# Performance work log

Hardware: AMD Instinct MI355X
Metric: run time of the kernel (lower is better)

Reference implementation:

```python
import jax, jax.numpy as jnp
import numpy as np

G = 16          # num graphs (equal-size contiguous segments)
P = 500         # kde_grid_points
Q = 20          # num quantiles, np.linspace(0,1,20)
SQRT2PI = float(np.sqrt(2.0 * np.pi))


def _gcn(x, src, dst, W, b):
    # PyG GCNConv: add self-loops, symmetric D^-1/2 (A+I) D^-1/2 aggregation.
    N = x.shape[0]
    xw = x @ W
    deg = jax.ops.segment_sum(jnp.ones_like(src, dtype=x.dtype), dst, num_segments=N) + 1.0
    dinv = jax.lax.rsqrt(deg)
    msg = xw[src] * (dinv[src] * dinv[dst])[:, None]            # [E, D]
    agg = jax.ops.segment_sum(msg, dst, num_segments=N) + xw * (dinv * dinv)[:, None]
    return agg + b


def _att_pool(x, Wg, bg):
    # GlobalAttention: softmax(gate_nn(x)) per graph, weighted sum of x.
    xg = x.reshape(G, -1, x.shape[-1])                          # [G, n, D]
    a = jax.nn.softmax(xg @ Wg + bg, axis=1)                    # [G, n, 1]
    return jnp.sum(a * xg, axis=1)                              # [G, D]


def _kde(xg):
    # xg: [n, D] nodes of one graph -> [D*Q] soft quantile features.
    quant = jnp.linspace(0.0, 1.0, Q, dtype=xg.dtype)
    n = xg.shape[0]
    mn = xg.min(axis=0) - 1e-6
    mx = xg.max(axis=0) + 1e-6
    grid = jnp.linspace(0.0, 1.0, P, dtype=xg.dtype)[:, None] * (mx - mn) + mn   # [P, D]
    std = xg.std(axis=0) + 1e-8 / 3                              # unbiased=False
    h = 1.06 * std * n ** (-0.2)                                 # Silverman bandwidth
    u = (grid[:, None, :] - xg[None, :, :]) / h                  # [P, n, D]
    kern = jnp.exp(-0.5 * u * u) / (h * SQRT2PI)
    dens = kern.mean(axis=1)                                     # [P, D]
    cdf = jnp.cumsum(dens, axis=0)
    cdf = cdf / jnp.clip(cdf[-1:], 1e-8)
    dist = jnp.abs(cdf[:, :, None] - quant)                      # [P, D, Q]
    w = jax.nn.sigmoid(-100.0 * dist)
    w = w / (w.sum(axis=0, keepdims=True) + 1e-8)
    return jnp.sum(grid[:, :, None] * w, axis=0).reshape(-1)     # [D*Q]


def setup_inputs() -> dict:
    key = jax.random.key(0)
    ks = jax.random.split(key, 26)
    N, E, D_in, D_h, D_out = 2048, 32768, 64, 64, 16
    rn = lambda k, s: jax.random.normal(k, s, jnp.float32) * 0.1
    return {
        'x': jax.random.normal(ks[0], (N, D_in), jnp.float32),
        'edge_index': jax.random.randint(ks[1], (2, E), 0, N),
        'gcn_W0': rn(ks[2], (D_in, D_h)), 'gcn_b0': rn(ks[3], (D_h,)),
        'gcn_W1': rn(ks[4], (D_h, D_h)), 'gcn_b1': rn(ks[5], (D_h,)),
        'lp_W0': rn(ks[6], (D_in, D_out)), 'lp_b0': rn(ks[7], (D_out,)),
        'lp_W1': rn(ks[8], (D_h, D_out)), 'lp_b1': rn(ks[9], (D_out,)),
        'cls_W': rn(ks[10], (D_h, D_out)), 'cls_b': rn(ks[11], (D_out,)),
        'kp_W0': rn(ks[12], (D_in * Q, D_out)), 'kp_b0': rn(ks[13], (D_out,)),
        'kp_W1': rn(ks[14], (D_h * Q, D_out)), 'kp_b1': rn(ks[15], (D_out,)),
        'gate_W0': rn(ks[16], (D_in, 1)), 'gate_b0': rn(ks[17], (1,)),
        'gate_W1': rn(ks[18], (D_h, 1)), 'gate_b1': rn(ks[19], (1,)),
        'gate_W2': rn(ks[20], (D_h, 1)), 'gate_b2': rn(ks[21], (1,)),
        'beta': jax.random.normal(ks[22], (D_out,), jnp.float32),
        'h0': jax.random.normal(ks[23], (1,), jnp.float32),
    }


def reference(x, edge_index, gcn_W0, gcn_b0, gcn_W1, gcn_b1, lp_W0, lp_b0, lp_W1, lp_b1,
              cls_W, cls_b, kp_W0, kp_b0, kp_W1, kp_b1, gate_W0, gate_b0, gate_W1, gate_b1,
              gate_W2, gate_b2, beta, h0):
    src, dst = edge_index[0], edge_index[1]
    gcn_p = [(gcn_W0, gcn_b0), (gcn_W1, gcn_b1)]
    lp = [(lp_W0, lp_b0), (lp_W1, lp_b1)]
    kp = [(kp_W0, kp_b0), (kp_W1, kp_b1)]
    gate = [(gate_W0, gate_b0), (gate_W1, gate_b1)]
    cur = x
    h_list, kde_list = [], []
    for i in range(2):  # n_layers (dropout is identity in eval)
        pooled = _att_pool(cur, *gate[i])                        # [G, D]
        h_list.append(pooled @ lp[i][0] + lp[i][1])              # [G, out]
        kf = jax.vmap(_kde)(cur.reshape(G, -1, cur.shape[-1]))   # [G, D*Q]
        kde_list.append(kf @ kp[i][0] + kp[i][1])
        cur = _gcn(cur, src, dst, *gcn_p[i])
    h_list.append(_att_pool(cur, gate_W2, gate_b2) @ cls_W + cls_b)
    main_out = jnp.stack(h_list).mean(axis=0)                    # [G, out]
    kde_out = jnp.stack(kde_list).mean(axis=0)
    return (main_out + kde_out) @ beta + h0                      # [G]
```

## Files before the change

kernel.cpp:

```cpp
#include <hip/hip_runtime.h>
#include <math.h>

#define NNODE 2048
#define NEDGE 32768
#define DD 64
#define GG 16
#define NPG 128
#define PP 500
#define QQ 20
#define CAP 64

__device__ __forceinline__ float fexp2(float x) { return __builtin_amdgcn_exp2f(x); }
__device__ __forceinline__ float frcp(float x)  { return __builtin_amdgcn_rcpf(x); }
__device__ __forceinline__ float frsq(float x)  { return __builtin_amdgcn_rsqf(x); }

struct __align__(8) f2 { float x, y; };

struct KdeS { f2 bc[NPG]; f2 cg[512]; float sred[8]; float wtot[8]; float kfv[QQ]; };
struct AttS { float sc[NPG]; float part[8][DD]; float pooled[DD]; };
struct XwS  { float Ws[DD][DD]; float xr[8][DD]; };
union SmemU { KdeS k; AttS a; XwS x; };

__global__ void k_fill(const int* __restrict__ ei, int* __restrict__ cnt,
                       int* __restrict__ csr) {
    int e = blockIdx.x * 256 + threadIdx.x;
    int s = ei[e], dstn = ei[NEDGE + e];
    int pos = atomicAdd(&cnt[dstn], 1);
    if (pos < CAP) csr[dstn * CAP + pos] = s;
}

__device__ __forceinline__ void att_pool(AttS& s, const float* __restrict__ xg,
                                         const float* __restrict__ gW, float gb) {
    int t = threadIdx.x, lane = t & 63, wid = t >> 6;
    int node = t >> 2, seg = t & 3;
    const float* row = xg + node * DD + seg * 16;
    const float* gw = gW + seg * 16;
    float v = 0.f;
    #pragma unroll
    for (int k = 0; k < 16; k++) v = fmaf(row[k], gw[k], v);
    v += __shfl_xor(v, 1);
    v += __shfl_xor(v, 2);
    if (seg == 0) s.sc[node] = v + gb;
    __syncthreads();
    if (wid == 0) {
        float v0 = s.sc[lane], v1 = s.sc[lane + 64];
        float m = fmaxf(v0, v1);
        for (int o = 32; o; o >>= 1) m = fmaxf(m, __shfl_xor(m, o));
        float e0 = __expf(v0 - m), e1 = __expf(v1 - m);
        float ssum = e0 + e1;
        for (int o = 32; o; o >>= 1) ssum += __shfl_xor(ssum, o);
        float inv = frcp(ssum);
        s.sc[lane] = e0 * inv;
        s.sc[lane + 64] = e1 * inv;
    }
    __syncthreads();
    int d2 = t & 63, ch = t >> 6;
    const float* base = xg + ch * 16 * DD + d2;
    const float* av = s.sc + ch * 16;
    float p = 0.f;
    #pragma unroll
    for (int i = 0; i < 16; i++) p = fmaf(av[i], base[i * DD], p);
    s.part[ch][d2] = p;
    __syncthreads();
    if (t < DD) {
        float pd = 0.f;
        #pragma unroll
        for (int c2 = 0; c2 < 8; c2++) pd += s.part[c2][t];
        s.pooled[t] = pd;
    }
    __syncthreads();
}

__global__ __launch_bounds__(512) void k_mega(
    const float* __restrict__ xin, const int* __restrict__ cnt,
    float* __restrict__ xwout, float* __restrict__ hb, float* __restrict__ kout,
    const float* __restrict__ gcnW,
    const float* __restrict__ gateW, const float* __restrict__ gateB,
    const float* __restrict__ lpW, const float* __restrict__ lpB,
    const float* __restrict__ kpW) {
    __shared__ SmemU sm;
    int b = blockIdx.x, t = threadIdx.x, lane = t & 63, wid = t >> 6;

    if (b < GG * DD) {
        int g = b >> 6, d = b & 63;
        const float* xg = xin + g * NPG * DD + d;
        float a = 0.f;
        if (t < NPG) a = xg[t * DD];
        if (wid < 2) {
            float mn = a, mx = a, smv = a;
            for (int o = 32; o; o >>= 1) {
                mn = fminf(mn, __shfl_xor(mn, o));
                mx = fmaxf(mx, __shfl_xor(mx, o));
                smv += __shfl_xor(smv, o);
            }
            if (lane == 0) {
                sm.k.sred[wid * 3 + 0] = mn;
                sm.k.sred[wid * 3 + 1] = mx;
                sm.k.sred[wid * 3 + 2] = smv;
            }
        }
        __syncthreads();
        float mn = fminf(sm.k.sred[0], sm.k.sred[3]) - 1e-6f;
        float mx = fmaxf(sm.k.sred[1], sm.k.sred[4]) + 1e-6f;
        float mean = (sm.k.sred[2] + sm.k.sred[5]) * (1.f / 128.f);
        if (wid < 2) {
            float dv = a - mean;
            float sq = dv * dv;
            for (int o = 32; o; o >>= 1) sq += __shfl_xor(sq, o);
            if (lane == 0) sm.k.sred[6 + wid] = sq;
        }
        __syncthreads();
        float var = fmaxf((sm.k.sred[6] + sm.k.sred[7]) * (1.f / 128.f), 0.f);
        float sd = sqrtf(var) + (1e-8f / 3.0f);
        float h = 0.4016648901252554f * sd;
        const float L2E = 1.4426950408889634f;
        float A = -0.5f * L2E * frcp(h * h);
        if (t < NPG) { f2 v; v.x = -2.f * A * a; v.y = A * a * a; sm.k.bc[t] = v; }
        __syncthreads();
        float step = (mx - mn) * (1.f / 499.f);
        float gp = fmaf(step, (float)t, mn);
        float gA = A * gp * gp;
        float ac0 = 0.f, ac1 = 0.f, ac2 = 0.f, ac3 = 0.f;
        #pragma unroll 8
        for (int j = 0; j < NPG; j += 4) {
            f2 b0 = sm.k.bc[j], b1 = sm.k.bc[j + 1], b2 = sm.k.bc[j + 2], b3 = sm.k.bc[j + 3];
            ac0 += fexp2(gA + fmaf(b0.x, gp, b0.y));
            ac1 += fexp2(gA + fmaf(b1.x, gp, b1.y));
            ac2 += fexp2(gA + fmaf(b2.x, gp, b2.y));
            ac3 += fexp2(gA + fmaf(b3.x, gp, b3.y));
        }
        float invnh = frcp(128.f * h * 2.5066282746310002f);
        float dens = (t < PP) ? ((ac0 + ac1) + (ac2 + ac3)) * invnh : 0.f;
        float sc2 = dens;
        for (int o = 1; o < 64; o <<= 1) {
            float u = __shfl_up(sc2, o);
            if (lane >= o) sc2 += u;
        }
        if (lane == 63) sm.k.wtot[wid] = sc2;
        __syncthreads();
        float offs = 0.f, total = 0.f;
        #pragma unroll
        for (int w = 0; w < 8; w++) {
            float wv = sm.k.wtot[w];
            if (w < wid) offs += wv;
            total += wv;
        }
        float c = (offs + sc2) * frcp(fmaxf(total, 1e-8f));
        f2 cgv; cgv.x = (t < PP) ? c : 4.0f; cgv.y = (t < PP) ? gp : 0.f;
        sm.k.cg[t] = cgv;
        __syncthreads();
        int grp = t >> 4, sub = t & 15;
        if (grp < QQ) {
            float qv = (float)grp * (1.f / 19.f);
            float sw0 = 0.f, sw1 = 0.f, sg0 = 0.f, sg1 = 0.f;
            #pragma unroll
            for (int i = 0; i < 32; i += 2) {
                f2 v0 = sm.k.cg[i * 16 + sub];
                f2 v1 = sm.k.cg[(i + 1) * 16 + sub];
                float e0 = fexp2(fabsf(v0.x - qv) * 144.26950408889634f);
                float e1 = fexp2(fabsf(v1.x - qv) * 144.26950408889634f);
                float w0 = frcp(1.f + e0), w1 = frcp(1.f + e1);
                sw0 += w0; sg0 = fmaf(w0, v0.y, sg0);
                sw1 += w1; sg1 = fmaf(w1, v1.y, sg1);
            }
            float sw = sw0 + sw1, sg = sg0 + sg1;
            #pragma unroll
            for (int o = 1; o < 16; o <<= 1) {
                sw += __shfl_xor(sw, o);
                sg += __shfl_xor(sg, o);
            }
            if (sub == 0) sm.k.kfv[grp] = sg * frcp(sw + 1e-8f);
        }
        __syncthreads();
        if (t < 16) {
            float v = 0.f;
            #pragma unroll
            for (int q = 0; q < QQ; q++) v = fmaf(sm.k.kfv[q], kpW[(d * QQ + q) * 16 + t], v);
            atomicAdd(&kout[g * 16 + t], v);
        }
    } else if (b < GG * DD + GG) {
        int g = b - GG * DD;
        att_pool(sm.a, xin + g * NPG * DD, gateW, gateB[0]);
        if (t < 16) {
            float o = lpB[t];
            #pragma unroll
            for (int d2 = 0; d2 < DD; d2++) o = fmaf(sm.a.pooled[d2], lpW[d2 * 16 + t], o);
            hb[g * 16 + t] = o;
        }
    } else {
        int rb = b - (GG * DD + GG);
        int r0 = rb * 8;
        for (int i = t; i < DD * DD; i += 512) sm.x.Ws[i >> 6][i & 63] = gcnW[i];
        sm.x.xr[wid][lane] = xin[(r0 + wid) * DD + lane];
        __syncthreads();
        float s = 0.f;
        #pragma unroll
        for (int k = 0; k < DD; k++) s = fmaf(sm.x.xr[wid][k], sm.x.Ws[k][lane], s);
        float di = frsq((float)cnt[r0 + wid] + 1.0f);
        xwout[(r0 + wid) * DD + lane] = s * di;
    }
}

__global__ __launch_bounds__(512) void k_gather(const int* __restrict__ cnt,
                                                const int* __restrict__ csr,
                                                const float* __restrict__ xw,
                                                const float* __restrict__ bvec,
                                                float* __restrict__ cur) {
    int t = threadIdx.x, lane = t & 63, wid = t >> 6;
    int n = blockIdx.x * 8 + wid;
    int ec = cnt[n];
    if (ec > CAP) ec = CAP;
    const int* lst = csr + n * CAP;
    float sum = 0.f;
    int j = 0;
    for (; j + 4 <= ec; j += 4) {
        int s0 = lst[j], s1 = lst[j + 1], s2 = lst[j + 2], s3 = lst[j + 3];
        sum += xw[s0 * DD + lane] + xw[s1 * DD + lane] + xw[s2 * DD + lane] + xw[s3 * DD + lane];
    }
    for (; j < ec; j++) sum += xw[lst[j] * DD + lane];
    float di = frsq((float)cnt[n] + 1.f);
    cur[n * DD + lane] = di * (sum + xw[n * DD + lane]) + bvec[lane];
}

__global__ __launch_bounds__(512) void k_fin(const float* __restrict__ cur2,
    const float* __restrict__ gW2, const float* __restrict__ gb2,
    const float* __restrict__ clsW, const float* __restrict__ clsB,
    const float* __restrict__ hb, const float* __restrict__ kout,
    const float* __restrict__ kpb0, const float* __restrict__ kpb1,
    const float* __restrict__ beta, const float* __restrict__ h0s,
    float* __restrict__ out) {
    __shared__ SmemU sm;
    __shared__ float red[16];
    int g = blockIdx.x, t = threadIdx.x;
    att_pool(sm.a, cur2 + g * NPG * DD, gW2, gb2[0]);
    if (t < 16) {
        float h2 = clsB[t];
        #pragma unroll
        for (int d2 = 0; d2 < DD; d2++) h2 = fmaf(sm.a.pooled[d2], clsW[d2 * 16 + t], h2);
        float mo = (hb[g * 16 + t] + hb[256 + g * 16 + t] + h2) * (1.f / 3.f);
        float ko = (kout[g * 16 + t] + kpb0[t] + kout[256 + g * 16 + t] + kpb1[t]) * 0.5f;
        red[t] = (mo + ko) * beta[t];
    }
    __syncthreads();
    if (t == 0) {
        float s = 0.f;
        #pragma unroll
        for (int j = 0; j < 16; j++) s += red[j];
        out[g] = s + h0s[0];
    }
}

extern "C" void kernel_launch(void* const* d_in, const int* in_sizes, int n_in,
                              void* d_out, int out_size, void* d_ws, size_t ws_size,
                              hipStream_t stream) {
    const float* x       = (const float*)d_in[0];
    const int*   ei      = (const int*)  d_in[1];
    const float* gcn_W0  = (const float*)d_in[2];
    const float* gcn_b0  = (const float*)d_in[3];
    const float* gcn_W1  = (const float*)d_in[4];
    const float* gcn_b1  = (const float*)d_in[5];
    const float* lp_W0   = (const float*)d_in[6];
    const float* lp_b0   = (const float*)d_in[7];
    const float* lp_W1   = (const float*)d_in[8];
    const float* lp_b1   = (const float*)d_in[9];
    const float* cls_W   = (const float*)d_in[10];
    const float* cls_b   = (const float*)d_in[11];
    const float* kp_W0   = (const float*)d_in[12];
    const float* kp_b0   = (const float*)d_in[13];
    const float* kp_W1   = (const float*)d_in[14];
    const float* kp_b1   = (const float*)d_in[15];
    const float* gate_W0 = (const float*)d_in[16];
    const float* gate_b0 = (const float*)d_in[17];
    const float* gate_W1 = (const float*)d_in[18];
    const float* gate_b1 = (const float*)d_in[19];
    const float* gate_W2 = (const float*)d_in[20];
    const float* gate_b2 = (const float*)d_in[21];
    const float* beta    = (const float*)d_in[22];
    const float* h0s     = (const float*)d_in[23];

    float* ws  = (float*)d_ws;
    int* cnt   = (int*)ws;
    float* kout = ws + 2048;
    int* csr   = (int*)(ws + 2560);
    float* A   = ws + 2560 + NNODE * CAP;
    float* B   = A + NNODE * DD;
    float* hb  = B + NNODE * DD;

    hipMemsetAsync(ws, 0, 2560 * sizeof(float), stream);

    k_fill<<<NEDGE / 256, 256, 0, stream>>>(ei, cnt, csr);

    k_mega<<<GG * DD + GG + NNODE / 8, 512, 0, stream>>>(
        x, cnt, A, hb, kout, gcn_W0, gate_W0, gate_b0, lp_W0, lp_b0, kp_W0);
    k_gather<<<NNODE / 8, 512, 0, stream>>>(cnt, csr, A, gcn_b0, B);

    k_mega<<<GG * DD + GG + NNODE / 8, 512, 0, stream>>>(
        B, cnt, A, hb + 256, kout + 256, gcn_W1, gate_W1, gate_b1, lp_W1, lp_b1, kp_W1);
    k_gather<<<NNODE / 8, 512, 0, stream>>>(cnt, csr, A, gcn_b1, B);

    k_fin<<<GG, 512, 0, stream>>>(B, gate_W2, gate_b2, cls_W, cls_b,
                                  hb, kout, kp_b0, kp_b1, beta, h0s, (float*)d_out);
}
```

Measured before the change: 66.45 us.

## Replace atomic KDE accumulation with per-block partials and swap memset for kernel

The per-dimension KDE blocks now write their projected 16-value contribution to a dedicated partial buffer instead of atomically adding into a shared output. The final kernel sums the 64 partials per graph, so the KDE output no longer needs zeroing, and the remaining zeroing of edge counts is done by a tiny kernel instead of a memset call. The change also vectorises the shared-memory bandwidth-coefficient reads and the weight tile load to float4, and splits the gather accumulator into two chains. This removes atomic contention and memset overhead at the cost of extra workspace and a serial 64-element reduction in the final kernel.

```diff
diff --git a/kernel.cpp b/kernel.cpp
--- a/kernel.cpp
+++ b/kernel.cpp
@@ -20,6 +20,10 @@
 struct AttS { float sc[NPG]; float part[8][DD]; float pooled[DD]; };
 struct XwS  { float Ws[DD][DD]; float xr[8][DD]; };
 union SmemU { KdeS k; AttS a; XwS x; };
+
+__global__ void k_zero(int* __restrict__ p) {
+    p[blockIdx.x * 512 + threadIdx.x] = 0;
+}
 
 __global__ void k_fill(const int* __restrict__ ei, int* __restrict__ cnt,
                        int* __restrict__ csr) {
@@ -73,7 +77,7 @@
 
 __global__ __launch_bounds__(512) void k_mega(
     const float* __restrict__ xin, const int* __restrict__ cnt,
-    float* __restrict__ xwout, float* __restrict__ hb, float* __restrict__ kout,
+    float* __restrict__ xwout, float* __restrict__ hb, float* __restrict__ kpart,
     const float* __restrict__ gcnW,
     const float* __restrict__ gateW, const float* __restrict__ gateB,
     const float* __restrict__ lpW, const float* __restrict__ lpB,
@@ -120,14 +124,15 @@
         float step = (mx - mn) * (1.f / 499.f);
         float gp = fmaf(step, (float)t, mn);
         float gA = A * gp * gp;
+        const float4* bc4 = (const float4*)sm.k.bc;
         float ac0 = 0.f, ac1 = 0.f, ac2 = 0.f, ac3 = 0.f;
-        #pragma unroll 8
-        for (int j = 0; j < NPG; j += 4) {
-            f2 b0 = sm.k.bc[j], b1 = sm.k.bc[j + 1], b2 = sm.k.bc[j + 2], b3 = sm.k.bc[j + 3];
-            ac0 += fexp2(gA + fmaf(b0.x, gp, b0.y));
-            ac1 += fexp2(gA + fmaf(b1.x, gp, b1.y));
-            ac2 += fexp2(gA + fmaf(b2.x, gp, b2.y));
-            ac3 += fexp2(gA + fmaf(b3.x, gp, b3.y));
+        #pragma unroll 4
+        for (int j4 = 0; j4 < 64; j4 += 2) {
+            float4 p = bc4[j4], q = bc4[j4 + 1];
+            ac0 += fexp2(gA + fmaf(p.x, gp, p.y));
+            ac1 += fexp2(gA + fmaf(p.z, gp, p.w));
+            ac2 += fexp2(gA + fmaf(q.x, gp, q.y));
+            ac3 += fexp2(gA + fmaf(q.z, gp, q.w));
         }
         float invnh = frcp(128.f * h * 2.5066282746310002f);
         float dens = (t < PP) ? ((ac0 + ac1) + (ac2 + ac3)) * invnh : 0.f;
@@ -176,7 +181,7 @@
             float v = 0.f;
             #pragma unroll
             for (int q = 0; q < QQ; q++) v = fmaf(sm.k.kfv[q], kpW[(d * QQ + q) * 16 + t], v);
-            atomicAdd(&kout[g * 16 + t], v);
+            kpart[b * 16 + t] = v;
         }
     } else if (b < GG * DD + GG) {
         int g = b - GG * DD;
@@ -190,7 +195,10 @@
     } else {
         int rb = b - (GG * DD + GG);
         int r0 = rb * 8;
-        for (int i = t; i < DD * DD; i += 512) sm.x.Ws[i >> 6][i & 63] = gcnW[i];
+        float4* Wv = (float4*)&sm.x.Ws[0][0];
+        const float4* Gv = (const float4*)gcnW;
+        Wv[t] = Gv[t];
+        Wv[t + 512] = Gv[t + 512];
         sm.x.xr[wid][lane] = xin[(r0 + wid) * DD + lane];
         __syncthreads();
         float s = 0.f;
@@ -211,21 +219,22 @@
     int ec = cnt[n];
     if (ec > CAP) ec = CAP;
     const int* lst = csr + n * CAP;
-    float sum = 0.f;
+    float sum0 = 0.f, sum1 = 0.f;
     int j = 0;
     for (; j + 4 <= ec; j += 4) {
         int s0 = lst[j], s1 = lst[j + 1], s2 = lst[j + 2], s3 = lst[j + 3];
-        sum += xw[s0 * DD + lane] + xw[s1 * DD + lane] + xw[s2 * DD + lane] + xw[s3 * DD + lane];
-    }
-    for (; j < ec; j++) sum += xw[lst[j] * DD + lane];
+        sum0 += xw[s0 * DD + lane] + xw[s1 * DD + lane];
+        sum1 += xw[s2 * DD + lane] + xw[s3 * DD + lane];
+    }
+    for (; j < ec; j++) sum0 += xw[lst[j] * DD + lane];
     float di = frsq((float)cnt[n] + 1.f);
-    cur[n * DD + lane] = di * (sum + xw[n * DD + lane]) + bvec[lane];
+    cur[n * DD + lane] = di * ((sum0 + sum1) + xw[n * DD + lane]) + bvec[lane];
 }
 
 __global__ __launch_bounds__(512) void k_fin(const float* __restrict__ cur2,
     const float* __restrict__ gW2, const float* __restrict__ gb2,
     const float* __restrict__ clsW, const float* __restrict__ clsB,
-    const float* __restrict__ hb, const float* __restrict__ kout,
+    const float* __restrict__ hb, const float* __restrict__ kpart,
     const float* __restrict__ kpb0, const float* __restrict__ kpb1,
     const float* __restrict__ beta, const float* __restrict__ h0s,
     float* __restrict__ out) {
@@ -237,8 +246,16 @@
         float h2 = clsB[t];
         #pragma unroll
         for (int d2 = 0; d2 < DD; d2++) h2 = fmaf(sm.a.pooled[d2], clsW[d2 * 16 + t], h2);
+        const float* kp0 = kpart + g * DD * 16 + t;
+        const float* kp1 = kp0 + GG * DD * 16;
+        float s0 = 0.f, s1 = 0.f;
+        #pragma unroll
+        for (int d2 = 0; d2 < DD; d2++) {
+            s0 += kp0[d2 * 16];
+            s1 += kp1[d2 * 16];
+        }
         float mo = (hb[g * 16 + t] + hb[256 + g * 16 + t] + h2) * (1.f / 3.f);
-        float ko = (kout[g * 16 + t] + kpb0[t] + kout[256 + g * 16 + t] + kpb1[t]) * 0.5f;
+        float ko = (s0 + kpb0[t] + s1 + kpb1[t]) * 0.5f;
         red[t] = (mo + ko) * beta[t];
     }
     __syncthreads();
@@ -280,24 +297,24 @@
 
     float* ws  = (float*)d_ws;
     int* cnt   = (int*)ws;
-    float* kout = ws + 2048;
-    int* csr   = (int*)(ws + 2560);
-    float* A   = ws + 2560 + NNODE * CAP;
+    int* csr   = (int*)(ws + 2048);
+    float* A   = ws + 2048 + NNODE * CAP;
     float* B   = A + NNODE * DD;
     float* hb  = B + NNODE * DD;
-
-    hipMemsetAsync(ws, 0, 2560 * sizeof(float), stream);
+    float* kp  = hb + 512;
+
+    k_zero<<<4, 512, 0, stream>>>(cnt);
 
     k_fill<<<NEDGE / 256, 256, 0, stream>>>(ei, cnt, csr);
 
     k_mega<<<GG * DD + GG + NNODE / 8, 512, 0, stream>>>(
-        x, cnt, A, hb, kout, gcn_W0, gate_W0, gate_b0, lp_W0, lp_b0, kp_W0);
+        x, cnt, A, hb, kp, gcn_W0, gate_W0, gate_b0, lp_W0, lp_b0, kp_W0);
     k_gather<<<NNODE / 8, 512, 0, stream>>>(cnt, csr, A, gcn_b0, B);
 
     k_mega<<<GG * DD + GG + NNODE / 8, 512, 0, stream>>>(
-        B, cnt, A, hb + 256, kout + 256, gcn_W1, gate_W1, gate_b1, lp_W1, lp_b1, kp_W1);
+        B, cnt, A, hb + 256, kp + GG * DD * 16, gcn_W1, gate_W1, gate_b1, lp_W1, lp_b1, kp_W1);
     k_gather<<<NNODE / 8, 512, 0, stream>>>(cnt, csr, A, gcn_b1, B);
 
     k_fin<<<GG, 512, 0, stream>>>(B, gate_W2, gate_b2, cls_W, cls_b,
-                                  hb, kout, kp_b0, kp_b1, beta, h0s, (float*)d_out);
-}
+                                  hb, kp, kp_b0, kp_b1, beta, h0s, (float*)d_out);
+}
```

Result: no change. 66.45 us (+0.0%).
